# Kernel tuning notes

Hardware: AMD Instinct MI355X
Metric: run time of the kernel (lower is better)

## Reference

```python
import jax, jax.numpy as jnp
import numpy as np

DIM = 512
HEADS = 8
DIM_HEAD = 32
INNER = HEADS * DIM_HEAD  # 256
B, N = 2, 2048
EPS = 1e-5


def setup_inputs() -> dict:
    key = jax.random.key(0)
    ks = jax.random.split(key, 6)
    x = jax.random.normal(ks[0], (B, N, DIM), dtype=jnp.float32)
    rel_pos_bias = jax.random.normal(ks[1], (HEADS, N, N), dtype=jnp.float32)
    ln_scale = jnp.ones((DIM,), dtype=jnp.float32)
    w_qkv = jax.random.normal(ks[2], (DIM, INNER * 3), dtype=jnp.float32) / np.sqrt(DIM)
    w_out = jax.random.normal(ks[3], (INNER, DIM), dtype=jnp.float32) / np.sqrt(INNER)
    b_out = jnp.zeros((DIM,), dtype=jnp.float32)
    return {"x": x, "rel_pos_bias": rel_pos_bias, "ln_scale": ln_scale,
            "w_qkv": w_qkv, "w_out": w_out, "b_out": b_out}


def reference(x, rel_pos_bias, ln_scale, w_qkv, w_out, b_out):
    scale = DIM_HEAD ** -0.5
    # LayerNorm (no bias), eps=1e-5
    mu = jnp.mean(x, axis=-1, keepdims=True)
    var = jnp.mean(jnp.square(x - mu), axis=-1, keepdims=True)
    xn = (x - mu) * jax.lax.rsqrt(var + EPS) * ln_scale
    # fused QKV projection, no bias
    qkv = xn @ w_qkv  # [b, n, 3*inner]
    q, k, v = jnp.split(qkv, 3, axis=-1)
    def to_heads(t):
        b, n, _ = t.shape
        return t.reshape(b, n, HEADS, DIM_HEAD).transpose(0, 2, 1, 3)  # b h n d
    q, k, v = map(to_heads, (q, k, v))
    q = q * scale
    sim = jnp.einsum('bhid,bhjd->bhij', q, k)
    sim = sim + rel_pos_bias  # (h,n,n) broadcasts over batch
    attn = jax.nn.softmax(sim, axis=-1)
    o = jnp.einsum('bhij,bhjd->bhid', attn, v)
    o = o.transpose(0, 2, 1, 3).reshape(x.shape[0], x.shape[1], INNER)  # b n (h d)
    return o @ w_out + b_out
```

## Files before the change

### kernel.cpp

```cpp
#include <hip/hip_runtime.h>
#include <hip/hip_bf16.h>
#include <cstdint>

#define NB 2
#define NSEQ 2048
#define NDIM 512
#define NHEAD 8
#define DHEAD 32
#define NINNER 256
#define NQKV 768
#define LNEPS 1e-5f
#define QSCALE 0.17677669529663687f

typedef short short8 __attribute__((ext_vector_type(8)));
typedef float f32x4 __attribute__((ext_vector_type(4)));
typedef unsigned short u16;
typedef unsigned int u32;

__device__ __forceinline__ f32x4 mfma16(short8 a, short8 b, f32x4 c) {
    return __builtin_amdgcn_mfma_f32_16x16x32_bf16(a, b, c, 0, 0, 0);
}

__device__ __forceinline__ u16 f2bf(float a) {
    union { float f; u32 u; } x; x.f = a;
    u32 r = x.u + 0x7fffu + ((x.u >> 16) & 1u);
    return (u16)(r >> 16);
}
__device__ __forceinline__ float bf2f(u16 h) {
    union { float f; u32 u; } x; x.u = ((u32)h) << 16; return x.f;
}
__device__ __forceinline__ void split2(float a, u16& hi, u16& lo) {
    hi = f2bf(a);
    lo = f2bf(a - bf2f(hi));
}

__global__ __launch_bounds__(256) void ln_kernel(
    const float* __restrict__ x, const float* __restrict__ gamma,
    u32* __restrict__ xn_hi, u32* __restrict__ xn_lo)
{
    const int row = blockIdx.x;
    const int t = threadIdx.x;
    const float2 v = ((const float2*)(x + (size_t)row * NDIM))[t];
    float s1 = v.x + v.y;
    float s2 = v.x * v.x + v.y * v.y;
    #pragma unroll
    for (int off = 32; off >= 1; off >>= 1) {
        s1 += __shfl_down(s1, off);
        s2 += __shfl_down(s2, off);
    }
    __shared__ float a1[4], a2[4];
    if ((t & 63) == 0) { a1[t >> 6] = s1; a2[t >> 6] = s2; }
    __syncthreads();
    const float ts1 = a1[0] + a1[1] + a1[2] + a1[3];
    const float ts2 = a2[0] + a2[1] + a2[2] + a2[3];
    const float mu = ts1 * (1.0f / NDIM);
    const float var = ts2 * (1.0f / NDIM) - mu * mu;
    const float rs = rsqrtf(var + LNEPS);
    const float2 g = ((const float2*)gamma)[t];
    const float xn0 = (v.x - mu) * rs * g.x;
    const float xn1 = (v.y - mu) * rs * g.y;
    u16 h0, l0, h1, l1;
    split2(xn0, h0, l0);
    split2(xn1, h1, l1);
    xn_hi[(size_t)row * (NDIM / 2) + t] = (u32)h0 | ((u32)h1 << 16);
    xn_lo[(size_t)row * (NDIM / 2) + t] = (u32)l0 | ((u32)l1 << 16);
}

__global__ __launch_bounds__(256) void wsplit_kernel(
    const float* __restrict__ w, u16* __restrict__ tT_hi, u16* __restrict__ tT_lo,
    int K, int Ncols)
{
    const int idx = blockIdx.x * 256 + threadIdx.x;
    const int k = idx / Ncols;
    const int n = idx - k * Ncols;
    u16 hh, ll;
    split2(w[idx], hh, ll);
    tT_hi[(size_t)n * K + k] = hh;
    tT_lo[(size_t)n * K + k] = ll;
}

__global__ __launch_bounds__(256, 4) void qkv_kernel(
    const u16* __restrict__ xn_hi, const u16* __restrict__ xn_lo,
    const u16* __restrict__ wT_hi, const u16* __restrict__ wT_lo,
    u16* __restrict__ q_hi, u16* __restrict__ q_lo,
    u16* __restrict__ k_hi, u16* __restrict__ k_lo,
    u16* __restrict__ vt_hi)
{
    const int t = threadIdx.x;
    const int wave = t >> 6, lane = t & 63;
    const int lrow = lane & 15, lquad = lane >> 4;
    const int rowBase = blockIdx.x * 64;
    const int colBase = blockIdx.y * 64;
    const int wm = (wave >> 1) * 32;
    const int wn = (wave & 1) * 32;
    const int kf = lquad * 8;
    const size_t arow0 = (size_t)(rowBase + wm + lrow) * NDIM;
    const size_t arow1 = (size_t)(rowBase + wm + 16 + lrow) * NDIM;
    const size_t brow0 = (size_t)(colBase + wn + lrow) * NDIM;
    const size_t brow1 = (size_t)(colBase + wn + 16 + lrow) * NDIM;
    const f32x4 zero = {0.f, 0.f, 0.f, 0.f};
    f32x4 acc00 = zero, acc01 = zero, acc10 = zero, acc11 = zero;

    for (int k0 = 0; k0 < NDIM; k0 += 32) {
        const short8 a0h = *(const short8*)(xn_hi + arow0 + k0 + kf);
        const short8 a0l = *(const short8*)(xn_lo + arow0 + k0 + kf);
        const short8 a1h = *(const short8*)(xn_hi + arow1 + k0 + kf);
        const short8 a1l = *(const short8*)(xn_lo + arow1 + k0 + kf);
        const short8 b0h = *(const short8*)(wT_hi + brow0 + k0 + kf);
        const short8 b0l = *(const short8*)(wT_lo + brow0 + k0 + kf);
        const short8 b1h = *(const short8*)(wT_hi + brow1 + k0 + kf);
        const short8 b1l = *(const short8*)(wT_lo + brow1 + k0 + kf);
        acc00 = mfma16(a0h, b0h, acc00); acc00 = mfma16(a0h, b0l, acc00); acc00 = mfma16(a0l, b0h, acc00);
        acc01 = mfma16(a0h, b1h, acc01); acc01 = mfma16(a0h, b1l, acc01); acc01 = mfma16(a0l, b1h, acc01);
        acc10 = mfma16(a1h, b0h, acc10); acc10 = mfma16(a1h, b0l, acc10); acc10 = mfma16(a1l, b0h, acc10);
        acc11 = mfma16(a1h, b1h, acc11); acc11 = mfma16(a1h, b1l, acc11); acc11 = mfma16(a1l, b1h, acc11);
    }

    #pragma unroll
    for (int mi = 0; mi < 2; mi++) {
        #pragma unroll
        for (int ni = 0; ni < 2; ni++) {
            f32x4 acc = (mi == 0) ? ((ni == 0) ? acc00 : acc01)
                                  : ((ni == 0) ? acc10 : acc11);
            #pragma unroll
            for (int r = 0; r < 4; r++) {
                const int grow = rowBase + wm + mi * 16 + lquad * 4 + r;
                const int gcol = colBase + wn + ni * 16 + lrow;
                const float v = acc[r];
                const int bidx = grow >> 11;
                const int n = grow & (NSEQ - 1);
                const int sec = gcol >> 8;
                const int idx = gcol & 255;
                const int head = idx >> 5, d = idx & 31;
                const int bh = bidx * NHEAD + head;
                if (sec == 0) {
                    u16 hh, ll;
                    split2(v * QSCALE, hh, ll);
                    const size_t a = ((size_t)bh * NSEQ + n) * DHEAD + d;
                    q_hi[a] = hh; q_lo[a] = ll;
                } else if (sec == 1) {
                    u16 hh, ll;
                    split2(v, hh, ll);
                    const size_t a = ((size_t)bh * NSEQ + n) * DHEAD + d;
                    k_hi[a] = hh; k_lo[a] = ll;
                } else {
                    const size_t a = ((size_t)bh * DHEAD + d) * NSEQ + n;
                    vt_hi[a] = f2bf(v);
                }
            }
        }
    }
}

__global__ __launch_bounds__(256, 6) void attn_kernel(
    const u16* __restrict__ q_hi, const u16* __restrict__ q_lo,
    const u16* __restrict__ k_hi, const u16* __restrict__ k_lo,
    const u16* __restrict__ vt_hi,
    const float* __restrict__ bias,
    u16* __restrict__ o_hi, u16* __restrict__ o_lo)
{
    __shared__ __align__(16) u16 Ph[4][16][40];
    __shared__ __align__(16) float cA[4][64][4];
    __shared__ __align__(16) float cB[4][64][4];
    __shared__ float cl[4][16];
    const int t = threadIdx.x;
    const int wave = t >> 6, lane = t & 63;
    const int lrow = lane & 15, lquad = lane >> 4;
    const int bh = blockIdx.y;
    const int head = bh & (NHEAD - 1);
    const int qb = blockIdx.x * 16;
    const size_t qkbase = (size_t)bh * NSEQ * DHEAD;
    const short8 qh = *(const short8*)(q_hi + qkbase + (size_t)(qb + lrow) * DHEAD + lquad * 8);
    const short8 ql = *(const short8*)(q_lo + qkbase + (size_t)(qb + lrow) * DHEAD + lquad * 8);
    const f32x4 zero = {0.f, 0.f, 0.f, 0.f};
    f32x4 accA = zero, accB = zero;
    float lp[4] = {0.f, 0.f, 0.f, 0.f};
    const float* biasrow = bias + (size_t)head * NSEQ * NSEQ + (size_t)(qb + lquad * 4) * NSEQ + lrow;
    const size_t vbase = (size_t)bh * DHEAD * NSEQ;
    const int ktbase = wave * 512;

    for (int i = 0; i < 16; i++) {
        const int kt = ktbase + i * 32;
        const short8 kh0 = *(const short8*)(k_hi + qkbase + (size_t)(kt + lrow) * DHEAD + lquad * 8);
        const short8 kl0 = *(const short8*)(k_lo + qkbase + (size_t)(kt + lrow) * DHEAD + lquad * 8);
        const short8 kh1 = *(const short8*)(k_hi + qkbase + (size_t)(kt + 16 + lrow) * DHEAD + lquad * 8);
        const short8 kl1 = *(const short8*)(k_lo + qkbase + (size_t)(kt + 16 + lrow) * DHEAD + lquad * 8);
        f32x4 s0 = zero, s1 = zero;
        s0 = mfma16(qh, kh0, s0); s0 = mfma16(qh, kl0, s0); s0 = mfma16(ql, kh0, s0);
        s1 = mfma16(qh, kh1, s1); s1 = mfma16(qh, kl1, s1); s1 = mfma16(ql, kh1, s1);
        #pragma unroll
        for (int r = 0; r < 4; r++) {
            const float p0 = __expf(s0[r] + biasrow[(size_t)r * NSEQ + kt]);
            const float p1 = __expf(s1[r] + biasrow[(size_t)r * NSEQ + kt + 16]);
            lp[r] += p0 + p1;
            Ph[wave][lquad * 4 + r][lrow] = f2bf(p0);
            Ph[wave][lquad * 4 + r][16 + lrow] = f2bf(p1);
        }
        const short8 ph = *(const short8*)&Ph[wave][lrow][lquad * 8];
        const short8 v0h = *(const short8*)(vt_hi + vbase + (size_t)lrow * NSEQ + kt + lquad * 8);
        const short8 v1h = *(const short8*)(vt_hi + vbase + (size_t)(16 + lrow) * NSEQ + kt + lquad * 8);
        accA = mfma16(ph, v0h, accA);
        accB = mfma16(ph, v1h, accB);
    }

    #pragma unroll
    for (int r = 0; r < 4; r++) {
        lp[r] += __shfl_xor(lp[r], 8);
        lp[r] += __shfl_xor(lp[r], 4);
        lp[r] += __shfl_xor(lp[r], 2);
        lp[r] += __shfl_xor(lp[r], 1);
    }
    *(f32x4*)&cA[wave][lane][0] = accA;
    *(f32x4*)&cB[wave][lane][0] = accB;
    if (lrow == 0) {
        #pragma unroll
        for (int r = 0; r < 4; r++) cl[wave][lquad * 4 + r] = lp[r];
    }
    __syncthreads();
    if (wave == 0) {
        f32x4 sA = *(const f32x4*)&cA[0][lane][0];
        f32x4 sB = *(const f32x4*)&cB[0][lane][0];
        #pragma unroll
        for (int w = 1; w < 4; w++) {
            sA += *(const f32x4*)&cA[w][lane][0];
            sB += *(const f32x4*)&cB[w][lane][0];
        }
        const int bidx = bh >> 3;
        #pragma unroll
        for (int r = 0; r < 4; r++) {
            const float lt = cl[0][lquad * 4 + r] + cl[1][lquad * 4 + r]
                           + cl[2][lquad * 4 + r] + cl[3][lquad * 4 + r];
            const float inv = 1.0f / lt;
            const int q = qb + lquad * 4 + r;
            const size_t base = ((size_t)bidx * NSEQ + q) * NINNER + head * DHEAD;
            u16 hh, ll;
            split2(sA[r] * inv, hh, ll);
            o_hi[base + lrow] = hh; o_lo[base + lrow] = ll;
            split2(sB[r] * inv, hh, ll);
            o_hi[base + 16 + lrow] = hh; o_lo[base + 16 + lrow] = ll;
        }
    }
}

__global__ __launch_bounds__(256, 4) void out_kernel(
    const u16* __restrict__ o_hi, const u16* __restrict__ o_lo,
    const u16* __restrict__ wT_hi, const u16* __restrict__ wT_lo,
    const float* __restrict__ b_out,
    float* __restrict__ out)
{
    const int t = threadIdx.x;
    const int wave = t >> 6, lane = t & 63;
    const int lrow = lane & 15, lquad = lane >> 4;
    const int rowBase = blockIdx.x * 64;
    const int colBase = blockIdx.y * 64;
    const int wm = (wave >> 1) * 32;
    const int wn = (wave & 1) * 32;
    const int kf = lquad * 8;
    const size_t arow0 = (size_t)(rowBase + wm + lrow) * NINNER;
    const size_t arow1 = (size_t)(rowBase + wm + 16 + lrow) * NINNER;
    const size_t brow0 = (size_t)(colBase + wn + lrow) * NINNER;
    const size_t brow1 = (size_t)(colBase + wn + 16 + lrow) * NINNER;
    const f32x4 zero = {0.f, 0.f, 0.f, 0.f};
    f32x4 acc00 = zero, acc01 = zero, acc10 = zero, acc11 = zero;

    for (int k0 = 0; k0 < NINNER; k0 += 32) {
        const short8 a0h = *(const short8*)(o_hi + arow0 + k0 + kf);
        const short8 a0l = *(const short8*)(o_lo + arow0 + k0 + kf);
        const short8 a1h = *(const short8*)(o_hi + arow1 + k0 + kf);
        const short8 a1l = *(const short8*)(o_lo + arow1 + k0 + kf);
        const short8 b0h = *(const short8*)(wT_hi + brow0 + k0 + kf);
        const short8 b0l = *(const short8*)(wT_lo + brow0 + k0 + kf);
        const short8 b1h = *(const short8*)(wT_hi + brow1 + k0 + kf);
        const short8 b1l = *(const short8*)(wT_lo + brow1 + k0 + kf);
        acc00 = mfma16(a0h, b0h, acc00); acc00 = mfma16(a0h, b0l, acc00); acc00 = mfma16(a0l, b0h, acc00);
        acc01 = mfma16(a0h, b1h, acc01); acc01 = mfma16(a0h, b1l, acc01); acc01 = mfma16(a0l, b1h, acc01);
        acc10 = mfma16(a1h, b0h, acc10); acc10 = mfma16(a1h, b0l, acc10); acc10 = mfma16(a1l, b0h, acc10);
        acc11 = mfma16(a1h, b1h, acc11); acc11 = mfma16(a1h, b1l, acc11); acc11 = mfma16(a1l, b1h, acc11);
    }

    #pragma unroll
    for (int mi = 0; mi < 2; mi++) {
        #pragma unroll
        for (int ni = 0; ni < 2; ni++) {
            f32x4 acc = (mi == 0) ? ((ni == 0) ? acc00 : acc01)
                                  : ((ni == 0) ? acc10 : acc11);
            #pragma unroll
            for (int r = 0; r < 4; r++) {
                const int grow = rowBase + wm + mi * 16 + lquad * 4 + r;
                const int gcol = colBase + wn + ni * 16 + lrow;
                out[(size_t)grow * NDIM + gcol] = acc[r] + b_out[gcol];
            }
        }
    }
}

extern "C" void kernel_launch(void* const* d_in, const int* in_sizes, int n_in,
                              void* d_out, int out_size, void* d_ws, size_t ws_size,
                              hipStream_t stream)
{
    (void)in_sizes; (void)n_in; (void)out_size; (void)ws_size;
    const float* x     = (const float*)d_in[0];
    const float* bias  = (const float*)d_in[1];
    const float* gamma = (const float*)d_in[2];
    const float* wqkv  = (const float*)d_in[3];
    const float* wout  = (const float*)d_in[4];
    const float* bout  = (const float*)d_in[5];
    float* out = (float*)d_out;

    char* ws = (char*)d_ws;
    size_t off = 0;
    auto carve = [&](size_t bytes) -> void* {
        void* p = (void*)(ws + off);
        off += (bytes + 255) & ~(size_t)255;
        return p;
    };
    const size_t rows = (size_t)NB * NSEQ;
    const size_t hn = (size_t)NB * NHEAD * NSEQ * DHEAD;
    u16* xn_hi = (u16*)carve(rows * NDIM * 2);
    u16* xn_lo = (u16*)carve(rows * NDIM * 2);
    u16* wqT_hi = (u16*)carve((size_t)NQKV * NDIM * 2);
    u16* wqT_lo = (u16*)carve((size_t)NQKV * NDIM * 2);
    u16* woT_hi = (u16*)carve((size_t)NDIM * NINNER * 2);
    u16* woT_lo = (u16*)carve((size_t)NDIM * NINNER * 2);
    u16* q_hi  = (u16*)carve(hn * 2);
    u16* q_lo  = (u16*)carve(hn * 2);
    u16* k_hi  = (u16*)carve(hn * 2);
    u16* k_lo  = (u16*)carve(hn * 2);
    u16* vt_hi = (u16*)carve(hn * 2);
    u16* o_hi  = (u16*)carve(rows * NINNER * 2);
    u16* o_lo  = (u16*)carve(rows * NINNER * 2);

    ln_kernel<<<dim3((unsigned)rows), 256, 0, stream>>>(x, gamma, (u32*)xn_hi, (u32*)xn_lo);
    wsplit_kernel<<<dim3((NDIM * NQKV) / 256), 256, 0, stream>>>(wqkv, wqT_hi, wqT_lo, NDIM, NQKV);
    wsplit_kernel<<<dim3((NINNER * NDIM) / 256), 256, 0, stream>>>(wout, woT_hi, woT_lo, NINNER, NDIM);
    qkv_kernel<<<dim3(64, 12), 256, 0, stream>>>(xn_hi, xn_lo, wqT_hi, wqT_lo,
                                                 q_hi, q_lo, k_hi, k_lo, vt_hi);
    attn_kernel<<<dim3(128, 16), 256, 0, stream>>>(q_hi, q_lo, k_hi, k_lo,
                                                   vt_hi, bias, o_hi, o_lo);
    out_kernel<<<dim3(64, 8), 256, 0, stream>>>(o_hi, o_lo, woT_hi, woT_lo, bout, out);
}
```

Baseline: 342.6 us.

## Share bias loads across batches in attention and LDS-tile the projection GEMMs

The attention kernel now handles both batch items for a given head in one block, so each rel_pos_bias element is read once instead of twice. It also loads the bias as float2 with a one-iteration prefetch and uses an even/odd key split so each lane packs two probabilities per LDS write. The QKV and output projection GEMMs now stage 128x32 A tiles and 64x32 B tiles in shared memory, and each wave computes a 64x32 sub-tile. This trades fewer blocks and higher register pressure (lower launch-bounds occupancy) for halved bias traffic and more operand reuse.

```diff
diff --git a/kernel.cpp b/kernel.cpp
--- a/kernel.cpp
+++ b/kernel.cpp
@@ -79,54 +79,66 @@
     tT_lo[(size_t)n * K + k] = ll;
 }
 
-__global__ __launch_bounds__(256, 4) void qkv_kernel(
+__global__ __launch_bounds__(256, 3) void qkv_kernel(
     const u16* __restrict__ xn_hi, const u16* __restrict__ xn_lo,
     const u16* __restrict__ wT_hi, const u16* __restrict__ wT_lo,
     u16* __restrict__ q_hi, u16* __restrict__ q_lo,
     u16* __restrict__ k_hi, u16* __restrict__ k_lo,
     u16* __restrict__ vt_hi)
 {
+    __shared__ __align__(16) u16 Ah[128][40], Al[128][40], Bh[64][40], Bl[64][40];
     const int t = threadIdx.x;
     const int wave = t >> 6, lane = t & 63;
     const int lrow = lane & 15, lquad = lane >> 4;
-    const int rowBase = blockIdx.x * 64;
+    const int rowBase = blockIdx.x * 128;
     const int colBase = blockIdx.y * 64;
-    const int wm = (wave >> 1) * 32;
-    const int wn = (wave & 1) * 32;
+    const int rm = (wave & 1) * 64;
+    const int cn = (wave >> 1) * 32;
     const int kf = lquad * 8;
-    const size_t arow0 = (size_t)(rowBase + wm + lrow) * NDIM;
-    const size_t arow1 = (size_t)(rowBase + wm + 16 + lrow) * NDIM;
-    const size_t brow0 = (size_t)(colBase + wn + lrow) * NDIM;
-    const size_t brow1 = (size_t)(colBase + wn + 16 + lrow) * NDIM;
     const f32x4 zero = {0.f, 0.f, 0.f, 0.f};
-    f32x4 acc00 = zero, acc01 = zero, acc10 = zero, acc11 = zero;
+    f32x4 acc[4][2];
+    #pragma unroll
+    for (int mi = 0; mi < 4; mi++) { acc[mi][0] = zero; acc[mi][1] = zero; }
+
+    const int ar0 = t >> 2, ac0 = (t & 3) * 8;
+    const int ar1 = (t + 256) >> 2, ac1 = ((t + 256) & 3) * 8;
+    const int br = t >> 2, bc = (t & 3) * 8;
 
     for (int k0 = 0; k0 < NDIM; k0 += 32) {
-        const short8 a0h = *(const short8*)(xn_hi + arow0 + k0 + kf);
-        const short8 a0l = *(const short8*)(xn_lo + arow0 + k0 + kf);
-        const short8 a1h = *(const short8*)(xn_hi + arow1 + k0 + kf);
-        const short8 a1l = *(const short8*)(xn_lo + arow1 + k0 + kf);
-        const short8 b0h = *(const short8*)(wT_hi + brow0 + k0 + kf);
-        const short8 b0l = *(const short8*)(wT_lo + brow0 + k0 + kf);
-        const short8 b1h = *(const short8*)(wT_hi + brow1 + k0 + kf);
-        const short8 b1l = *(const short8*)(wT_lo + brow1 + k0 + kf);
-        acc00 = mfma16(a0h, b0h, acc00); acc00 = mfma16(a0h, b0l, acc00); acc00 = mfma16(a0l, b0h, acc00);
-        acc01 = mfma16(a0h, b1h, acc01); acc01 = mfma16(a0h, b1l, acc01); acc01 = mfma16(a0l, b1h, acc01);
-        acc10 = mfma16(a1h, b0h, acc10); acc10 = mfma16(a1h, b0l, acc10); acc10 = mfma16(a1l, b0h, acc10);
-        acc11 = mfma16(a1h, b1h, acc11); acc11 = mfma16(a1h, b1l, acc11); acc11 = mfma16(a1l, b1h, acc11);
-    }
-
-    #pragma unroll
-    for (int mi = 0; mi < 2; mi++) {
+        __syncthreads();
+        *(short8*)&Ah[ar0][ac0] = *(const short8*)(xn_hi + (size_t)(rowBase + ar0) * NDIM + k0 + ac0);
+        *(short8*)&Al[ar0][ac0] = *(const short8*)(xn_lo + (size_t)(rowBase + ar0) * NDIM + k0 + ac0);
+        *(short8*)&Ah[ar1][ac1] = *(const short8*)(xn_hi + (size_t)(rowBase + ar1) * NDIM + k0 + ac1);
+        *(short8*)&Al[ar1][ac1] = *(const short8*)(xn_lo + (size_t)(rowBase + ar1) * NDIM + k0 + ac1);
+        *(short8*)&Bh[br][bc] = *(const short8*)(wT_hi + (size_t)(colBase + br) * NDIM + k0 + bc);
+        *(short8*)&Bl[br][bc] = *(const short8*)(wT_lo + (size_t)(colBase + br) * NDIM + k0 + bc);
+        __syncthreads();
+        const short8 b0h = *(const short8*)&Bh[cn + lrow][kf];
+        const short8 b0l = *(const short8*)&Bl[cn + lrow][kf];
+        const short8 b1h = *(const short8*)&Bh[cn + 16 + lrow][kf];
+        const short8 b1l = *(const short8*)&Bl[cn + 16 + lrow][kf];
+        #pragma unroll
+        for (int mi = 0; mi < 4; mi++) {
+            const short8 ah = *(const short8*)&Ah[rm + mi * 16 + lrow][kf];
+            const short8 al = *(const short8*)&Al[rm + mi * 16 + lrow][kf];
+            acc[mi][0] = mfma16(ah, b0h, acc[mi][0]);
+            acc[mi][0] = mfma16(ah, b0l, acc[mi][0]);
+            acc[mi][0] = mfma16(al, b0h, acc[mi][0]);
+            acc[mi][1] = mfma16(ah, b1h, acc[mi][1]);
+            acc[mi][1] = mfma16(ah, b1l, acc[mi][1]);
+            acc[mi][1] = mfma16(al, b1h, acc[mi][1]);
+        }
+    }
+
+    #pragma unroll
+    for (int mi = 0; mi < 4; mi++) {
         #pragma unroll
         for (int ni = 0; ni < 2; ni++) {
-            f32x4 acc = (mi == 0) ? ((ni == 0) ? acc00 : acc01)
-                                  : ((ni == 0) ? acc10 : acc11);
             #pragma unroll
             for (int r = 0; r < 4; r++) {
-                const int grow = rowBase + wm + mi * 16 + lquad * 4 + r;
-                const int gcol = colBase + wn + ni * 16 + lrow;
-                const float v = acc[r];
+                const int grow = rowBase + rm + mi * 16 + lquad * 4 + r;
+                const int gcol = colBase + cn + ni * 16 + lrow;
+                const float v = acc[mi][ni][r];
                 const int bidx = grow >> 11;
                 const int n = grow & (NSEQ - 1);
                 const int sec = gcol >> 8;
@@ -152,7 +164,7 @@
     }
 }
 
-__global__ __launch_bounds__(256, 6) void attn_kernel(
+__global__ __launch_bounds__(256, 4) void attn_kernel(
     const u16* __restrict__ q_hi, const u16* __restrict__ q_lo,
     const u16* __restrict__ k_hi, const u16* __restrict__ k_lo,
     const u16* __restrict__ vt_hi,
@@ -160,79 +172,126 @@
     u16* __restrict__ o_hi, u16* __restrict__ o_lo)
 {
     __shared__ __align__(16) u16 Ph[4][16][40];
-    __shared__ __align__(16) float cA[4][64][4];
-    __shared__ __align__(16) float cB[4][64][4];
-    __shared__ float cl[4][16];
+    __shared__ __align__(16) float cA[2][4][64][4];
+    __shared__ __align__(16) float cB[2][4][64][4];
+    __shared__ float cl[2][4][16];
     const int t = threadIdx.x;
     const int wave = t >> 6, lane = t & 63;
     const int lrow = lane & 15, lquad = lane >> 4;
-    const int bh = blockIdx.y;
-    const int head = bh & (NHEAD - 1);
+    const int head = blockIdx.y;
     const int qb = blockIdx.x * 16;
-    const size_t qkbase = (size_t)bh * NSEQ * DHEAD;
-    const short8 qh = *(const short8*)(q_hi + qkbase + (size_t)(qb + lrow) * DHEAD + lquad * 8);
-    const short8 ql = *(const short8*)(q_lo + qkbase + (size_t)(qb + lrow) * DHEAD + lquad * 8);
+    const size_t qk0 = (size_t)head * NSEQ * DHEAD;
+    const size_t qk1 = (size_t)(NHEAD + head) * NSEQ * DHEAD;
+    const short8 qh0 = *(const short8*)(q_hi + qk0 + (size_t)(qb + lrow) * DHEAD + lquad * 8);
+    const short8 ql0 = *(const short8*)(q_lo + qk0 + (size_t)(qb + lrow) * DHEAD + lquad * 8);
+    const short8 qh1 = *(const short8*)(q_hi + qk1 + (size_t)(qb + lrow) * DHEAD + lquad * 8);
+    const short8 ql1 = *(const short8*)(q_lo + qk1 + (size_t)(qb + lrow) * DHEAD + lquad * 8);
     const f32x4 zero = {0.f, 0.f, 0.f, 0.f};
-    f32x4 accA = zero, accB = zero;
-    float lp[4] = {0.f, 0.f, 0.f, 0.f};
-    const float* biasrow = bias + (size_t)head * NSEQ * NSEQ + (size_t)(qb + lquad * 4) * NSEQ + lrow;
-    const size_t vbase = (size_t)bh * DHEAD * NSEQ;
-    const int ktbase = wave * 512;
+    f32x4 accA0 = zero, accB0 = zero, accA1 = zero, accB1 = zero;
+    float lp0[4] = {0.f, 0.f, 0.f, 0.f};
+    float lp1[4] = {0.f, 0.f, 0.f, 0.f};
+    const float* biasrow = bias + (size_t)head * NSEQ * NSEQ + (size_t)(qb + lquad * 4) * NSEQ;
+    const int kt0 = wave * 512;
+
+    float2 bq[4];
+    #pragma unroll
+    for (int r = 0; r < 4; r++)
+        bq[r] = *(const float2*)(biasrow + (size_t)r * NSEQ + kt0 + 2 * lrow);
 
     for (int i = 0; i < 16; i++) {
-        const int kt = ktbase + i * 32;
-        const short8 kh0 = *(const short8*)(k_hi + qkbase + (size_t)(kt + lrow) * DHEAD + lquad * 8);
-        const short8 kl0 = *(const short8*)(k_lo + qkbase + (size_t)(kt + lrow) * DHEAD + lquad * 8);
-        const short8 kh1 = *(const short8*)(k_hi + qkbase + (size_t)(kt + 16 + lrow) * DHEAD + lquad * 8);
-        const short8 kl1 = *(const short8*)(k_lo + qkbase + (size_t)(kt + 16 + lrow) * DHEAD + lquad * 8);
-        f32x4 s0 = zero, s1 = zero;
-        s0 = mfma16(qh, kh0, s0); s0 = mfma16(qh, kl0, s0); s0 = mfma16(ql, kh0, s0);
-        s1 = mfma16(qh, kh1, s1); s1 = mfma16(qh, kl1, s1); s1 = mfma16(ql, kh1, s1);
+        const int kt = kt0 + i * 32;
+        const int ktn = kt0 + ((i + 1) & 15) * 32;
+        const size_t ke = (size_t)(kt + 2 * lrow) * DHEAD + lquad * 8;
+        const short8 kh0e = *(const short8*)(k_hi + qk0 + ke);
+        const short8 kl0e = *(const short8*)(k_lo + qk0 + ke);
+        const short8 kh0o = *(const short8*)(k_hi + qk0 + ke + DHEAD);
+        const short8 kl0o = *(const short8*)(k_lo + qk0 + ke + DHEAD);
+        const short8 kh1e = *(const short8*)(k_hi + qk1 + ke);
+        const short8 kl1e = *(const short8*)(k_lo + qk1 + ke);
+        const short8 kh1o = *(const short8*)(k_hi + qk1 + ke + DHEAD);
+        const short8 kl1o = *(const short8*)(k_lo + qk1 + ke + DHEAD);
+        const short8 v00 = *(const short8*)(vt_hi + qk0 + (size_t)lrow * NSEQ + kt + lquad * 8);
+        const short8 v01 = *(const short8*)(vt_hi + qk0 + (size_t)(16 + lrow) * NSEQ + kt + lquad * 8);
+        const short8 v10 = *(const short8*)(vt_hi + qk1 + (size_t)lrow * NSEQ + kt + lquad * 8);
+        const short8 v11 = *(const short8*)(vt_hi + qk1 + (size_t)(16 + lrow) * NSEQ + kt + lquad * 8);
+        float2 bn[4];
+        #pragma unroll
+        for (int r = 0; r < 4; r++)
+            bn[r] = *(const float2*)(biasrow + (size_t)r * NSEQ + ktn + 2 * lrow);
+        f32x4 s0 = zero, s1 = zero, u0 = zero, u1 = zero;
+        s0 = mfma16(qh0, kh0e, s0); s0 = mfma16(qh0, kl0e, s0); s0 = mfma16(ql0, kh0e, s0);
+        s1 = mfma16(qh0, kh0o, s1); s1 = mfma16(qh0, kl0o, s1); s1 = mfma16(ql0, kh0o, s1);
+        u0 = mfma16(qh1, kh1e, u0); u0 = mfma16(qh1, kl1e, u0); u0 = mfma16(ql1, kh1e, u0);
+        u1 = mfma16(qh1, kh1o, u1); u1 = mfma16(qh1, kl1o, u1); u1 = mfma16(ql1, kh1o, u1);
         #pragma unroll
         for (int r = 0; r < 4; r++) {
-            const float p0 = __expf(s0[r] + biasrow[(size_t)r * NSEQ + kt]);
-            const float p1 = __expf(s1[r] + biasrow[(size_t)r * NSEQ + kt + 16]);
-            lp[r] += p0 + p1;
-            Ph[wave][lquad * 4 + r][lrow] = f2bf(p0);
-            Ph[wave][lquad * 4 + r][16 + lrow] = f2bf(p1);
-        }
-        const short8 ph = *(const short8*)&Ph[wave][lrow][lquad * 8];
-        const short8 v0h = *(const short8*)(vt_hi + vbase + (size_t)lrow * NSEQ + kt + lquad * 8);
-        const short8 v1h = *(const short8*)(vt_hi + vbase + (size_t)(16 + lrow) * NSEQ + kt + lquad * 8);
-        accA = mfma16(ph, v0h, accA);
-        accB = mfma16(ph, v1h, accB);
+            const float p0 = __expf(s0[r] + bq[r].x);
+            const float p1 = __expf(s1[r] + bq[r].y);
+            lp0[r] += p0 + p1;
+            const u32 pk = (u32)f2bf(p0) | ((u32)f2bf(p1) << 16);
+            *(u32*)&Ph[wave][lquad * 4 + r][2 * lrow] = pk;
+        }
+        {
+            const short8 ph = *(const short8*)&Ph[wave][lrow][lquad * 8];
+            accA0 = mfma16(ph, v00, accA0);
+            accB0 = mfma16(ph, v01, accB0);
+        }
+        #pragma unroll
+        for (int r = 0; r < 4; r++) {
+            const float p0 = __expf(u0[r] + bq[r].x);
+            const float p1 = __expf(u1[r] + bq[r].y);
+            lp1[r] += p0 + p1;
+            const u32 pk = (u32)f2bf(p0) | ((u32)f2bf(p1) << 16);
+            *(u32*)&Ph[wave][lquad * 4 + r][2 * lrow] = pk;
+        }
+        {
+            const short8 ph = *(const short8*)&Ph[wave][lrow][lquad * 8];
+            accA1 = mfma16(ph, v10, accA1);
+            accB1 = mfma16(ph, v11, accB1);
+        }
+        #pragma unroll
+        for (int r = 0; r < 4; r++) bq[r] = bn[r];
     }
 
     #pragma unroll
     for (int r = 0; r < 4; r++) {
-        lp[r] += __shfl_xor(lp[r], 8);
-        lp[r] += __shfl_xor(lp[r], 4);
-        lp[r] += __shfl_xor(lp[r], 2);
-        lp[r] += __shfl_xor(lp[r], 1);
-    }
-    *(f32x4*)&cA[wave][lane][0] = accA;
-    *(f32x4*)&cB[wave][lane][0] = accB;
+        lp0[r] += __shfl_xor(lp0[r], 8);
+        lp0[r] += __shfl_xor(lp0[r], 4);
+        lp0[r] += __shfl_xor(lp0[r], 2);
+        lp0[r] += __shfl_xor(lp0[r], 1);
+        lp1[r] += __shfl_xor(lp1[r], 8);
+        lp1[r] += __shfl_xor(lp1[r], 4);
+        lp1[r] += __shfl_xor(lp1[r], 2);
+        lp1[r] += __shfl_xor(lp1[r], 1);
+    }
+    *(f32x4*)&cA[0][wave][lane][0] = accA0;
+    *(f32x4*)&cB[0][wave][lane][0] = accB0;
+    *(f32x4*)&cA[1][wave][lane][0] = accA1;
+    *(f32x4*)&cB[1][wave][lane][0] = accB1;
     if (lrow == 0) {
         #pragma unroll
-        for (int r = 0; r < 4; r++) cl[wave][lquad * 4 + r] = lp[r];
+        for (int r = 0; r < 4; r++) {
+            cl[0][wave][lquad * 4 + r] = lp0[r];
+            cl[1][wave][lquad * 4 + r] = lp1[r];
+        }
     }
     __syncthreads();
-    if (wave == 0) {
-        f32x4 sA = *(const f32x4*)&cA[0][lane][0];
-        f32x4 sB = *(const f32x4*)&cB[0][lane][0];
+    if (wave < 2) {
+        const int b = wave;
+        f32x4 sA = *(const f32x4*)&cA[b][0][lane][0];
+        f32x4 sB = *(const f32x4*)&cB[b][0][lane][0];
         #pragma unroll
         for (int w = 1; w < 4; w++) {
-            sA += *(const f32x4*)&cA[w][lane][0];
-            sB += *(const f32x4*)&cB[w][lane][0];
-        }
-        const int bidx = bh >> 3;
+            sA += *(const f32x4*)&cA[b][w][lane][0];
+            sB += *(const f32x4*)&cB[b][w][lane][0];
+        }
         #pragma unroll
         for (int r = 0; r < 4; r++) {
-            const float lt = cl[0][lquad * 4 + r] + cl[1][lquad * 4 + r]
-                           + cl[2][lquad * 4 + r] + cl[3][lquad * 4 + r];
+            const float lt = cl[b][0][lquad * 4 + r] + cl[b][1][lquad * 4 + r]
+                           + cl[b][2][lquad * 4 + r] + cl[b][3][lquad * 4 + r];
             const float inv = 1.0f / lt;
             const int q = qb + lquad * 4 + r;
-            const size_t base = ((size_t)bidx * NSEQ + q) * NINNER + head * DHEAD;
+            const size_t base = ((size_t)b * NSEQ + q) * NINNER + head * DHEAD;
             u16 hh, ll;
             split2(sA[r] * inv, hh, ll);
             o_hi[base + lrow] = hh; o_lo[base + lrow] = ll;
@@ -242,53 +301,65 @@
     }
 }
 
-__global__ __launch_bounds__(256, 4) void out_kernel(
+__global__ __launch_bounds__(256, 3) void out_kernel(
     const u16* __restrict__ o_hi, const u16* __restrict__ o_lo,
     const u16* __restrict__ wT_hi, const u16* __restrict__ wT_lo,
     const float* __restrict__ b_out,
     float* __restrict__ out)
 {
+    __shared__ __align__(16) u16 Ah[128][40], Al[128][40], Bh[64][40], Bl[64][40];
     const int t = threadIdx.x;
     const int wave = t >> 6, lane = t & 63;
     const int lrow = lane & 15, lquad = lane >> 4;
-    const int rowBase = blockIdx.x * 64;
+    const int rowBase = blockIdx.x * 128;
     const int colBase = blockIdx.y * 64;
-    const int wm = (wave >> 1) * 32;
-    const int wn = (wave & 1) * 32;
+    const int rm = (wave & 1) * 64;
+    const int cn = (wave >> 1) * 32;
     const int kf = lquad * 8;
-    const size_t arow0 = (size_t)(rowBase + wm + lrow) * NINNER;
-    const size_t arow1 = (size_t)(rowBase + wm + 16 + lrow) * NINNER;
-    const size_t brow0 = (size_t)(colBase + wn + lrow) * NINNER;
-    const size_t brow1 = (size_t)(colBase + wn + 16 + lrow) * NINNER;
     const f32x4 zero = {0.f, 0.f, 0.f, 0.f};
-    f32x4 acc00 = zero, acc01 = zero, acc10 = zero, acc11 = zero;
+    f32x4 acc[4][2];
+    #pragma unroll
+    for (int mi = 0; mi < 4; mi++) { acc[mi][0] = zero; acc[mi][1] = zero; }
+
+    const int ar0 = t >> 2, ac0 = (t & 3) * 8;
+    const int ar1 = (t + 256) >> 2, ac1 = ((t + 256) & 3) * 8;
+    const int br = t >> 2, bc = (t & 3) * 8;
 
     for (int k0 = 0; k0 < NINNER; k0 += 32) {
-        const short8 a0h = *(const short8*)(o_hi + arow0 + k0 + kf);
-        const short8 a0l = *(const short8*)(o_lo + arow0 + k0 + kf);
-        const short8 a1h = *(const short8*)(o_hi + arow1 + k0 + kf);
-        const short8 a1l = *(const short8*)(o_lo + arow1 + k0 + kf);
-        const short8 b0h = *(const short8*)(wT_hi + brow0 + k0 + kf);
-        const short8 b0l = *(const short8*)(wT_lo + brow0 + k0 + kf);
-        const short8 b1h = *(const short8*)(wT_hi + brow1 + k0 + kf);
-        const short8 b1l = *(const short8*)(wT_lo + brow1 + k0 + kf);
-        acc00 = mfma16(a0h, b0h, acc00); acc00 = mfma16(a0h, b0l, acc00); acc00 = mfma16(a0l, b0h, acc00);
-        acc01 = mfma16(a0h, b1h, acc01); acc01 = mfma16(a0h, b1l, acc01); acc01 = mfma16(a0l, b1h, acc01);
-        acc10 = mfma16(a1h, b0h, acc10); acc10 = mfma16(a1h, b0l, acc10); acc10 = mfma16(a1l, b0h, acc10);
-        acc11 = mfma16(a1h, b1h, acc11); acc11 = mfma16(a1h, b1l, acc11); acc11 = mfma16(a1l, b1h, acc11);
-    }
-
-    #pragma unroll
-    for (int mi = 0; mi < 2; mi++) {
+        __syncthreads();
+        *(short8*)&Ah[ar0][ac0] = *(const short8*)(o_hi + (size_t)(rowBase + ar0) * NINNER + k0 + ac0);
+        *(short8*)&Al[ar0][ac0] = *(const short8*)(o_lo + (size_t)(rowBase + ar0) * NINNER + k0 + ac0);
+        *(short8*)&Ah[ar1][ac1] = *(const short8*)(o_hi + (size_t)(rowBase + ar1) * NINNER + k0 + ac1);
+        *(short8*)&Al[ar1][ac1] = *(const short8*)(o_lo + (size_t)(rowBase + ar1) * NINNER + k0 + ac1);
+        *(short8*)&Bh[br][bc] = *(const short8*)(wT_hi + (size_t)(colBase + br) * NINNER + k0 + bc);
+        *(short8*)&Bl[br][bc] = *(const short8*)(wT_lo + (size_t)(colBase + br) * NINNER + k0 + bc);
+        __syncthreads();
+        const short8 b0h = *(const short8*)&Bh[cn + lrow][kf];
+        const short8 b0l = *(const short8*)&Bl[cn + lrow][kf];
+        const short8 b1h = *(const short8*)&Bh[cn + 16 + lrow][kf];
+        const short8 b1l = *(const short8*)&Bl[cn + 16 + lrow][kf];
+        #pragma unroll
+        for (int mi = 0; mi < 4; mi++) {
+            const short8 ah = *(const short8*)&Ah[rm + mi * 16 + lrow][kf];
+            const short8 al = *(const short8*)&Al[rm + mi * 16 + lrow][kf];
+            acc[mi][0] = mfma16(ah, b0h, acc[mi][0]);
+            acc[mi][0] = mfma16(ah, b0l, acc[mi][0]);
+            acc[mi][0] = mfma16(al, b0h, acc[mi][0]);
+            acc[mi][1] = mfma16(ah, b1h, acc[mi][1]);
+            acc[mi][1] = mfma16(ah, b1l, acc[mi][1]);
+            acc[mi][1] = mfma16(al, b1h, acc[mi][1]);
+        }
+    }
+
+    #pragma unroll
+    for (int mi = 0; mi < 4; mi++) {
         #pragma unroll
         for (int ni = 0; ni < 2; ni++) {
-            f32x4 acc = (mi == 0) ? ((ni == 0) ? acc00 : acc01)
-                                  : ((ni == 0) ? acc10 : acc11);
             #pragma unroll
             for (int r = 0; r < 4; r++) {
-                const int grow = rowBase + wm + mi * 16 + lquad * 4 + r;
-                const int gcol = colBase + wn + ni * 16 + lrow;
-                out[(size_t)grow * NDIM + gcol] = acc[r] + b_out[gcol];
+                const int grow = rowBase + rm + mi * 16 + lquad * 4 + r;
+                const int gcol = colBase + cn + ni * 16 + lrow;
+                out[(size_t)grow * NDIM + gcol] = acc[mi][ni][r] + b_out[gcol];
             }
         }
     }
@@ -333,9 +404,9 @@
     ln_kernel<<<dim3((unsigned)rows), 256, 0, stream>>>(x, gamma, (u32*)xn_hi, (u32*)xn_lo);
     wsplit_kernel<<<dim3((NDIM * NQKV) / 256), 256, 0, stream>>>(wqkv, wqT_hi, wqT_lo, NDIM, NQKV);
     wsplit_kernel<<<dim3((NINNER * NDIM) / 256), 256, 0, stream>>>(wout, woT_hi, woT_lo, NINNER, NDIM);
-    qkv_kernel<<<dim3(64, 12), 256, 0, stream>>>(xn_hi, xn_lo, wqT_hi, wqT_lo,
+    qkv_kernel<<<dim3(32, 12), 256, 0, stream>>>(xn_hi, xn_lo, wqT_hi, wqT_lo,
                                                  q_hi, q_lo, k_hi, k_lo, vt_hi);
-    attn_kernel<<<dim3(128, 16), 256, 0, stream>>>(q_hi, q_lo, k_hi, k_lo,
-                                                   vt_hi, bias, o_hi, o_lo);
-    out_kernel<<<dim3(64, 8), 256, 0, stream>>>(o_hi, o_lo, woT_hi, woT_lo, bout, out);
-}
+    attn_kernel<<<dim3(128, 8), 256, 0, stream>>>(q_hi, q_lo, k_hi, k_lo,
+                                                  vt_hi, bias, o_hi, o_lo);
+    out_kernel<<<dim3(32, 8), 256, 0, stream>>>(o_hi, o_lo, woT_hi, woT_lo, bout, out);
+}
```

New measurement: 331.1 us. 1.03x faster.
